# Kernel optimization log

Measured on AMD Instinct MI355X. Metric: run time of the kernel, lower is better.

## Reference

```python
import jax, jax.numpy as jnp
import numpy as np

B, C, H, W = 32, 512, 32, 32
N_WORDS, WORD_DIM = 77, 256
HW2 = H * W


def setup_inputs() -> dict:
    key = jax.random.key(0)
    k1, k2, k3 = jax.random.split(key, 3)
    feat = jax.random.normal(k1, (B, C, H, W), dtype=jnp.float32)
    word_emb = jax.random.normal(k2, (B, N_WORDS, WORD_DIM), dtype=jnp.float32)
    # nn.Linear(word_dim, img_hw*img_hw): weight (out,in), bias (out,)
    W_fc = jax.random.normal(k3, (HW2, WORD_DIM), dtype=jnp.float32) * (1.0 / np.sqrt(WORD_DIM))
    b_fc = jnp.zeros((HW2,), dtype=jnp.float32)
    return {"feat": feat, "word_emb": word_emb, "W_fc": W_fc, "b_fc": b_fc}


def reference(feat, word_emb, W_fc, b_fc):
    b, c, h, w = feat.shape
    f = feat.reshape(b, c, h * w)                                   # (b, c, hw2)
    we = jnp.einsum('bnd,kd->bnk', word_emb, W_fc) + b_fc           # (b, n, hw2)
    we = jnp.swapaxes(we, 1, 2)                                     # (b, hw2, n)
    scores = jnp.einsum('bck,bkn->bcn', f, we)                      # (b, c, n)
    att = jax.nn.softmax(scores, axis=-1)                           # (b, c, n)
    att_feat = jnp.einsum('bcn,bkn->bck', att, we)                  # (b, c, hw2)
    return att_feat.reshape(b, c, h, w)
```

## Files before the change

kernel.cpp:

```cpp
#include <hip/hip_runtime.h>

#define B_    32
#define C_    512
#define HW2_  1024
#define NW    77
#define NP    80
#define NPT   96
#define WD    256

typedef unsigned int   uint32;
typedef unsigned short u16;
typedef __attribute__((ext_vector_type(8))) short bf16x8;
typedef __attribute__((ext_vector_type(4))) float f32x4;

#define MFMA(a, b, c) __builtin_amdgcn_mfma_f32_16x16x32_bf16(a, b, c, 0, 0, 0)
#define SWALL() __builtin_amdgcn_sched_barrier(0)

#define WE_ELN   ((size_t)B_ * 16 * NP * 8)
#define WET_ELN  ((size_t)B_ * HW2_ * 12)

__device__ __forceinline__ void split1(float x, u16 &h, u16 &l) {
    uint32 u = __float_as_uint(x);
    h = (u16)(u >> 16);
    float r = x - __uint_as_float(u & 0xffff0000u);
    uint32 v = __float_as_uint(r);
    l = (u16)((v + 0x7fffu + ((v >> 16) & 1u)) >> 16);
}

__device__ __forceinline__ void split8(float4 a, float4 b, bf16x8 &h, bf16x8 &l) {
    float v[8] = {a.x, a.y, a.z, a.w, b.x, b.y, b.z, b.w};
    #pragma unroll
    for (int i = 0; i < 8; ++i) {
        u16 hh, ll; split1(v[i], hh, ll);
        h[i] = (short)hh; l[i] = (short)ll;
    }
}

__global__ __launch_bounds__(512, 4) void we_gemm(
    const float* __restrict__ word_emb, const float* __restrict__ W_fc,
    const float* __restrict__ b_fc,
    bf16x8* __restrict__ we_hi, bf16x8* __restrict__ we_lo,
    bf16x8* __restrict__ weT_hi, bf16x8* __restrict__ weT_lo)
{
    __shared__ __align__(16) uint32 HL[NP][68];

    const int id = blockIdx.x;
    const int b  = (id & 7) + 8 * (id >> 7);
    const int q  = (id >> 3) & 15;
    const int kb = q * 64;
    const int t  = threadIdx.x;
    const int h  = t >> 6;
    const int w  = h & 3, nh = h >> 2;
    const int lane = t & 63, lr = lane & 15, lg = lane >> 4;
    const int kout = kb + 16 * w + lr;
    const int m0 = nh ? 3 : 0;
    const int mc = nh ? 2 : 3;

    const float* wrow = W_fc + kout * WD;
    bf16x8 bh[8], bl[8];
    #pragma unroll
    for (int c = 0; c < 2; ++c) {
        float4 wx[4], wy[4];
        #pragma unroll
        for (int i = 0; i < 4; ++i) {
            const int dk = (c * 4 + i) * 32 + 8 * lg;
            wx[i] = *(const float4*)(wrow + dk);
            wy[i] = *(const float4*)(wrow + dk + 4);
        }
        SWALL();
        #pragma unroll
        for (int i = 0; i < 4; ++i) split8(wx[i], wy[i], bh[c * 4 + i], bl[c * 4 + i]);
    }

    f32x4 acc[3];
    #pragma unroll
    for (int mm = 0; mm < 3; ++mm) acc[mm] = (f32x4)0.0f;

    const float* emb = word_emb + b * NW * WD;

    #pragma unroll
    for (int ks = 0; ks < 8; ++ks) {
        const int dk = ks * 32 + 8 * lg;
        bf16x8 ah[3], al[3];
        #pragma unroll
        for (int mm = 0; mm < 3; ++mm) {
            if (mm < mc) {
                const int n = 16 * (m0 + mm) + lr;
                float4 x = make_float4(0.f, 0.f, 0.f, 0.f), y = x;
                if (n < NW) {
                    const float* p = emb + n * WD + dk;
                    x = *(const float4*)p; y = *(const float4*)(p + 4);
                }
                split8(x, y, ah[mm], al[mm]);
            }
        }
        #pragma unroll
        for (int mm = 0; mm < 3; ++mm) {
            if (mm < mc) {
                acc[mm] = MFMA(ah[mm], bh[ks], acc[mm]);
                acc[mm] = MFMA(ah[mm], bl[ks], acc[mm]);
                acc[mm] = MFMA(al[mm], bh[ks], acc[mm]);
                acc[mm] = MFMA(al[mm], bl[ks], acc[mm]);
            }
        }
    }

    const float bias = b_fc[kout];
    #pragma unroll
    for (int mm = 0; mm < 3; ++mm) {
        if (mm < mc) {
            #pragma unroll
            for (int r = 0; r < 4; ++r) {
                u16 hh, ll; split1(acc[mm][r] + bias, hh, ll);
                HL[16 * (m0 + mm) + 4 * lg + r][16 * w + lr] = ((uint32)hh << 16) | ll;
            }
        }
    }
    __syncthreads();

    for (int u = t; u < 640; u += 512) {
        const int n = u >> 3, c8 = (u & 7) * 8;
        uint4 p0 = *(const uint4*)&HL[n][c8];
        uint4 p1 = *(const uint4*)&HL[n][c8 + 4];
        const uint32 pw[8] = {p0.x, p0.y, p0.z, p0.w, p1.x, p1.y, p1.z, p1.w};
        bf16x8 hv, lv;
        #pragma unroll
        for (int i = 0; i < 8; ++i) {
            hv[i] = (short)(pw[i] >> 16);
            lv[i] = (short)(pw[i] & 0xffffu);
        }
        const int o = ((b * 16 + q) * NP + n) * 8 + (u & 7);
        we_hi[o] = hv; we_lo[o] = lv;
    }
    #pragma unroll
    for (int v0 = 0; v0 < 1536; v0 += 512) {
        const int v = v0 + t;
        const int sel = v >= 768;
        const int r2  = sel ? v - 768 : v;
        const int row = r2 / 12, g = r2 % 12;
        bf16x8 val;
        #pragma unroll
        for (int i = 0; i < 8; ++i) {
            const int n = g * 8 + i;
            const uint32 p = (n < NP) ? HL[n][row] : 0u;
            val[i] = (short)(sel ? (p & 0xffffu) : (p >> 16));
        }
        (sel ? weT_lo : weT_hi)[(b * HW2_ + kb + row) * 12 + g] = val;
    }
}

__global__ __launch_bounds__(512, 4) void attn_mfma(
    const float* __restrict__ feat,
    const bf16x8* __restrict__ we_hi, const bf16x8* __restrict__ we_lo,
    const bf16x8* __restrict__ weT_hi, const bf16x8* __restrict__ weT_lo,
    float* __restrict__ out)
{
    __shared__ __align__(16) float S[8][16][84];
    __shared__ __align__(16) u16   Ph[32][NPT];
    __shared__ __align__(16) u16   Pl[32][NPT];

    const int id  = blockIdx.x;
    const int b   = (id & 7) + 8 * (id >> 7);
    const int c0  = ((id >> 3) & 15) * 32;

    const int t    = threadIdx.x;
    const int h    = t >> 6;
    const int lane = t & 63, lr = lane & 15, lg = lane >> 4;

    const float* frow0 = feat + (size_t)(b * C_ + c0 + lr) * HW2_;
    const float* frow1 = frow0 + 16 * HW2_;

    f32x4 acc[2][5];
    #pragma unroll
    for (int s = 0; s < 2; ++s)
        #pragma unroll
        for (int m = 0; m < 5; ++m) acc[s][m] = (f32x4)0.0f;

    #pragma unroll
    for (int ks = 0; ks < 4; ++ks) {
        const int kk = h * 128 + ks * 32 + 8 * lg;
        bf16x8 fh0, fl0, fh1, fl1;
        {   float4 x = *(const float4*)(frow0 + kk);
            float4 y = *(const float4*)(frow0 + kk + 4);
            split8(x, y, fh0, fl0); }
        {   float4 x = *(const float4*)(frow1 + kk);
            float4 y = *(const float4*)(frow1 + kk + 4);
            split8(x, y, fh1, fl1); }
        const int qb  = (b * 16 + 2 * h + (ks >> 1)) * NP;
        const int sub = (ks & 1) * 4 + lg;
        #pragma unroll
        for (int m = 0; m < 5; ++m) {
            const int o = (qb + 16 * m + lr) * 8 + sub;
            const bf16x8 ah = we_hi[o];
            const bf16x8 al = we_lo[o];
            acc[0][m] = MFMA(ah, fh0, acc[0][m]);
            acc[0][m] = MFMA(ah, fl0, acc[0][m]);
            acc[0][m] = MFMA(al, fh0, acc[0][m]);
            acc[1][m] = MFMA(ah, fh1, acc[1][m]);
            acc[1][m] = MFMA(ah, fl1, acc[1][m]);
            acc[1][m] = MFMA(al, fh1, acc[1][m]);
        }
    }

    #pragma unroll
    for (int s = 0; s < 2; ++s) {
        #pragma unroll
        for (int m = 0; m < 5; ++m)
            #pragma unroll
            for (int r = 0; r < 4; ++r)
                S[h][lr][16 * m + 4 * lg + r] = acc[s][m][r];
        __syncthreads();
        {
            const int srow = 2 * h + (lane >> 5), col0 = lane & 31;
            float v3[3];
            float mx = -3.0e38f;
            #pragma unroll
            for (int j = 0; j < 3; ++j) {
                const int n = col0 + 32 * j;
                float sv = S[0][srow][n] + S[1][srow][n] + S[2][srow][n] + S[3][srow][n]
                         + S[4][srow][n] + S[5][srow][n] + S[6][srow][n] + S[7][srow][n];
                if (n < NW) mx = fmaxf(mx, sv);
                v3[j] = sv;
            }
            mx = fmaxf(mx, __shfl_xor(mx, 1));
            mx = fmaxf(mx, __shfl_xor(mx, 2));
            mx = fmaxf(mx, __shfl_xor(mx, 4));
            mx = fmaxf(mx, __shfl_xor(mx, 8));
            mx = fmaxf(mx, __shfl_xor(mx, 16));
            float sum = 0.f;
            #pragma unroll
            for (int j = 0; j < 3; ++j) {
                const int n = col0 + 32 * j;
                const float e = (n < NW) ? __expf(v3[j] - mx) : 0.f;
                v3[j] = e; sum += e;
            }
            sum += __shfl_xor(sum, 1);
            sum += __shfl_xor(sum, 2);
            sum += __shfl_xor(sum, 4);
            sum += __shfl_xor(sum, 8);
            sum += __shfl_xor(sum, 16);
            const float inv = 1.0f / sum;
            #pragma unroll
            for (int j = 0; j < 3; ++j) {
                const int n = col0 + 32 * j;
                u16 ph, pl; split1(v3[j] * inv, ph, pl);
                Ph[16 * s + srow][n] = ph; Pl[16 * s + srow][n] = pl;
            }
        }
        __syncthreads();
    }

    bf16x8 pbh[2][3], pbl[2][3];
    #pragma unroll
    for (int s = 0; s < 2; ++s)
        #pragma unroll
        for (int ksn = 0; ksn < 3; ++ksn) {
            pbh[s][ksn] = *(const bf16x8*)&Ph[16 * s + lr][32 * ksn + 8 * lg];
            pbl[s][ksn] = *(const bf16x8*)&Pl[16 * s + lr][32 * ksn + 8 * lg];
        }
    const bf16x8* th = weT_hi + (size_t)b * HW2_ * 12;
    const bf16x8* tl = weT_lo + (size_t)b * HW2_ * 12;
    float* orow0 = out + (size_t)(b * C_ + c0 + lr) * HW2_;
    float* orow1 = orow0 + 16 * HW2_;

    #pragma unroll
    for (int tt = 0; tt < 8; ++tt) {
        const int row = h * 128 + tt * 16 + lr;
        bf16x8 wa[3], wb[3];
        #pragma unroll
        for (int ksn = 0; ksn < 3; ++ksn) {
            wa[ksn] = th[row * 12 + 4 * ksn + lg];
            wb[ksn] = tl[row * 12 + 4 * ksn + lg];
        }
        f32x4 o0 = (f32x4)0.0f, o1 = (f32x4)0.0f;
        #pragma unroll
        for (int ksn = 0; ksn < 3; ++ksn) {
            o0 = MFMA(wa[ksn], pbh[0][ksn], o0);
            o0 = MFMA(wa[ksn], pbl[0][ksn], o0);
            o0 = MFMA(wb[ksn], pbh[0][ksn], o0);
            o1 = MFMA(wa[ksn], pbh[1][ksn], o1);
            o1 = MFMA(wa[ksn], pbl[1][ksn], o1);
            o1 = MFMA(wb[ksn], pbh[1][ksn], o1);
        }
        const int col = h * 128 + tt * 16 + 4 * lg;
        *(float4*)(orow0 + col) = make_float4(o0[0], o0[1], o0[2], o0[3]);
        *(float4*)(orow1 + col) = make_float4(o1[0], o1[1], o1[2], o1[3]);
    }
}

extern "C" void kernel_launch(void* const* d_in, const int* in_sizes, int n_in,
                              void* d_out, int out_size, void* d_ws, size_t ws_size,
                              hipStream_t stream) {
    (void)in_sizes; (void)n_in; (void)out_size; (void)ws_size;
    const float* feat     = (const float*)d_in[0];
    const float* word_emb = (const float*)d_in[1];
    const float* W_fc     = (const float*)d_in[2];
    const float* b_fc     = (const float*)d_in[3];

    bf16x8* we_hi  = (bf16x8*)d_ws;
    bf16x8* we_lo  = we_hi  + WE_ELN;
    bf16x8* weT_hi = we_lo  + WE_ELN;
    bf16x8* weT_lo = weT_hi + WET_ELN;

    we_gemm<<<512, 512, 0, stream>>>(word_emb, W_fc, b_fc, we_hi, we_lo, weT_hi, weT_lo);
    attn_mfma<<<512, 512, 0, stream>>>(feat, we_hi, we_lo, weT_hi, weT_lo, (float*)d_out);
}
```

Baseline: 179.4 us.

## Software-pipeline global loads in attention kernel with inline asm and manual vmcnt waits

Replaces the compiler-scheduled loads in the score GEMM and output GEMM phases with inline-asm global_load_dwordx4 issued several stages ahead into rotating register slots. Explicit s_waitcnt vmcnt counts and sched barriers let MFMA work overlap with outstanding memory loads. Launch bounds drop from 4 to 2 blocks per SM to make room for the extra registers, which lowers occupancy. Hand-counted vmcnt values are fragile, and any miscount (for example interleaved stores in phase 3 that also increment vmcnt) could cause races or over-waiting.

```diff
diff --git a/kernel.cpp b/kernel.cpp
--- a/kernel.cpp
+++ b/kernel.cpp
@@ -15,6 +15,10 @@
 
 #define MFMA(a, b, c) __builtin_amdgcn_mfma_f32_16x16x32_bf16(a, b, c, 0, 0, 0)
 #define SWALL() __builtin_amdgcn_sched_barrier(0)
+
+#define GLD4(dst, ptr) asm volatile("global_load_dwordx4 %0, %1, off" \
+                                    : "=v"(dst) : "v"(ptr))
+#define VMWAIT(n) asm volatile("s_waitcnt vmcnt(" #n ")" ::: "memory")
 
 #define WE_ELN   ((size_t)B_ * 16 * NP * 8)
 #define WET_ELN  ((size_t)B_ * HW2_ * 12)
@@ -149,7 +153,7 @@
     }
 }
 
-__global__ __launch_bounds__(512, 4) void attn_mfma(
+__global__ __launch_bounds__(512, 2) void attn_mfma(
     const float* __restrict__ feat,
     const bf16x8* __restrict__ we_hi, const bf16x8* __restrict__ we_lo,
     const bf16x8* __restrict__ weT_hi, const bf16x8* __restrict__ weT_lo,
@@ -170,37 +174,51 @@
     const float* frow0 = feat + (size_t)(b * C_ + c0 + lr) * HW2_;
     const float* frow1 = frow0 + 16 * HW2_;
 
+    float4 F[3][4];
+    bf16x8 WH[3][5], WL[3][5];
+
+#define P1_ISS(sl, ksv) do {                                        \
+        const int kk_ = h * 128 + (ksv) * 32 + 8 * lg;              \
+        GLD4(F[sl][0], frow0 + kk_);                                \
+        GLD4(F[sl][1], frow0 + kk_ + 4);                            \
+        GLD4(F[sl][2], frow1 + kk_);                                \
+        GLD4(F[sl][3], frow1 + kk_ + 4);                            \
+        const int qb_  = (b * 16 + 2 * h + ((ksv) >> 1)) * NP;      \
+        const int sub_ = ((ksv) & 1) * 4 + lg;                      \
+        _Pragma("unroll")                                           \
+        for (int m_ = 0; m_ < 5; ++m_) {                            \
+            GLD4(WH[sl][m_], we_hi + (qb_ + 16 * m_ + lr) * 8 + sub_); \
+            GLD4(WL[sl][m_], we_lo + (qb_ + 16 * m_ + lr) * 8 + sub_); \
+        } } while (0)
+
     f32x4 acc[2][5];
     #pragma unroll
     for (int s = 0; s < 2; ++s)
         #pragma unroll
         for (int m = 0; m < 5; ++m) acc[s][m] = (f32x4)0.0f;
 
-    #pragma unroll
-    for (int ks = 0; ks < 4; ++ks) {
-        const int kk = h * 128 + ks * 32 + 8 * lg;
-        bf16x8 fh0, fl0, fh1, fl1;
-        {   float4 x = *(const float4*)(frow0 + kk);
-            float4 y = *(const float4*)(frow0 + kk + 4);
-            split8(x, y, fh0, fl0); }
-        {   float4 x = *(const float4*)(frow1 + kk);
-            float4 y = *(const float4*)(frow1 + kk + 4);
-            split8(x, y, fh1, fl1); }
-        const int qb  = (b * 16 + 2 * h + (ks >> 1)) * NP;
-        const int sub = (ks & 1) * 4 + lg;
-        #pragma unroll
-        for (int m = 0; m < 5; ++m) {
-            const int o = (qb + 16 * m + lr) * 8 + sub;
-            const bf16x8 ah = we_hi[o];
-            const bf16x8 al = we_lo[o];
-            acc[0][m] = MFMA(ah, fh0, acc[0][m]);
-            acc[0][m] = MFMA(ah, fl0, acc[0][m]);
-            acc[0][m] = MFMA(al, fh0, acc[0][m]);
-            acc[1][m] = MFMA(ah, fh1, acc[1][m]);
-            acc[1][m] = MFMA(ah, fl1, acc[1][m]);
-            acc[1][m] = MFMA(al, fh1, acc[1][m]);
-        }
-    }
+#define P1_COMP(sl) do {                                            \
+        bf16x8 fh0, fl0, fh1, fl1;                                  \
+        split8(F[sl][0], F[sl][1], fh0, fl0);                       \
+        split8(F[sl][2], F[sl][3], fh1, fl1);                       \
+        _Pragma("unroll")                                           \
+        for (int m_ = 0; m_ < 5; ++m_) {                            \
+            acc[0][m_] = MFMA(WH[sl][m_], fh0, acc[0][m_]);         \
+            acc[0][m_] = MFMA(WH[sl][m_], fl0, acc[0][m_]);         \
+            acc[0][m_] = MFMA(WL[sl][m_], fh0, acc[0][m_]);         \
+            acc[1][m_] = MFMA(WH[sl][m_], fh1, acc[1][m_]);         \
+            acc[1][m_] = MFMA(WH[sl][m_], fl1, acc[1][m_]);         \
+            acc[1][m_] = MFMA(WL[sl][m_], fh1, acc[1][m_]);         \
+        } } while (0)
+
+    P1_ISS(0, 0);
+    P1_ISS(1, 1);
+    P1_ISS(2, 2); VMWAIT(28); SWALL(); P1_COMP(0);
+    P1_ISS(0, 3); VMWAIT(28); SWALL(); P1_COMP(1);
+    VMWAIT(14);   SWALL();             P1_COMP(2);
+    VMWAIT(0);    SWALL();             P1_COMP(0);
+#undef P1_ISS
+#undef P1_COMP
 
     #pragma unroll
     for (int s = 0; s < 2; ++s) {
@@ -263,29 +281,42 @@
     float* orow0 = out + (size_t)(b * C_ + c0 + lr) * HW2_;
     float* orow1 = orow0 + 16 * HW2_;
 
-    #pragma unroll
-    for (int tt = 0; tt < 8; ++tt) {
-        const int row = h * 128 + tt * 16 + lr;
-        bf16x8 wa[3], wb[3];
-        #pragma unroll
-        for (int ksn = 0; ksn < 3; ++ksn) {
-            wa[ksn] = th[row * 12 + 4 * ksn + lg];
-            wb[ksn] = tl[row * 12 + 4 * ksn + lg];
-        }
-        f32x4 o0 = (f32x4)0.0f, o1 = (f32x4)0.0f;
-        #pragma unroll
-        for (int ksn = 0; ksn < 3; ++ksn) {
-            o0 = MFMA(wa[ksn], pbh[0][ksn], o0);
-            o0 = MFMA(wa[ksn], pbl[0][ksn], o0);
-            o0 = MFMA(wb[ksn], pbh[0][ksn], o0);
-            o1 = MFMA(wa[ksn], pbh[1][ksn], o1);
-            o1 = MFMA(wa[ksn], pbl[1][ksn], o1);
-            o1 = MFMA(wb[ksn], pbh[1][ksn], o1);
-        }
-        const int col = h * 128 + tt * 16 + 4 * lg;
-        *(float4*)(orow0 + col) = make_float4(o0[0], o0[1], o0[2], o0[3]);
-        *(float4*)(orow1 + col) = make_float4(o1[0], o1[1], o1[2], o1[3]);
-    }
+    bf16x8 wa[2][3], wb[2][3];
+#define P3_ISS(sl, ttv) do {                                        \
+        const int row_ = h * 128 + (ttv) * 16 + lr;                 \
+        _Pragma("unroll")                                           \
+        for (int k_ = 0; k_ < 3; ++k_) {                            \
+            GLD4(wa[sl][k_], th + row_ * 12 + 4 * k_ + lg);         \
+            GLD4(wb[sl][k_], tl + row_ * 12 + 4 * k_ + lg);         \
+        } } while (0)
+
+#define P3_COMP(sl, ttv) do {                                       \
+        f32x4 o0 = (f32x4)0.0f, o1 = (f32x4)0.0f;                   \
+        _Pragma("unroll")                                           \
+        for (int ksn = 0; ksn < 3; ++ksn) {                         \
+            o0 = MFMA(wa[sl][ksn], pbh[0][ksn], o0);                \
+            o0 = MFMA(wa[sl][ksn], pbl[0][ksn], o0);                \
+            o0 = MFMA(wb[sl][ksn], pbh[0][ksn], o0);                \
+            o1 = MFMA(wa[sl][ksn], pbh[1][ksn], o1);                \
+            o1 = MFMA(wa[sl][ksn], pbl[1][ksn], o1);                \
+            o1 = MFMA(wb[sl][ksn], pbh[1][ksn], o1);                \
+        }                                                           \
+        const int col_ = h * 128 + (ttv) * 16 + 4 * lg;             \
+        *(float4*)(orow0 + col_) = make_float4(o0[0], o0[1], o0[2], o0[3]); \
+        *(float4*)(orow1 + col_) = make_float4(o1[0], o1[1], o1[2], o1[3]); \
+        } while (0)
+
+    P3_ISS(0, 0);
+    P3_ISS(1, 1); VMWAIT(6); SWALL(); P3_COMP(0, 0);
+    P3_ISS(0, 2); VMWAIT(8); SWALL(); P3_COMP(1, 1);
+    P3_ISS(1, 3); VMWAIT(8); SWALL(); P3_COMP(0, 2);
+    P3_ISS(0, 4); VMWAIT(8); SWALL(); P3_COMP(1, 3);
+    P3_ISS(1, 5); VMWAIT(8); SWALL(); P3_COMP(0, 4);
+    P3_ISS(0, 6); VMWAIT(8); SWALL(); P3_COMP(1, 5);
+    P3_ISS(1, 7); VMWAIT(8); SWALL(); P3_COMP(0, 6);
+    VMWAIT(2);    SWALL();            P3_COMP(1, 7);
+#undef P3_ISS
+#undef P3_COMP
 }
 
 extern "C" void kernel_launch(void* const* d_in, const int* in_sizes, int n_in,
```

Measured after the change: 186.3 us. 3.8% more time.
